# Kernel optimization log

Measured on AMD Instinct MI355X. Metric: run time of the kernel, lower is better.

Reference implementation:

```python
import jax, jax.numpy as jnp
import numpy as np

# Constants from the source's eval path
BBOX_STDS = (0.1, 0.1, 0.2, 0.2)   # cfg.TRAIN.BBOX_NORMALIZE_STDS (MEANS are zeros)
PRE_NMS = 300                       # cfg.TEST.RPN_POST_NMS_TOP_N
POST_K = 100                        # cfg.PERSON_NMS (fixed output size; zero-padded)
NMS_THRESH = 0.3
SCORE_THRESH = 0.05


def setup_inputs() -> dict:
    key = jax.random.key(0)
    k1, k2, k3, k4 = jax.random.split(key, 4)
    B, N = 64, 32768
    H = W = 1024.0
    # plausible RPN proposal boxes inside the image
    xy = jax.random.uniform(k1, (B, N, 2)) * (W - 160.0)
    wh = jax.random.uniform(k2, (B, N, 2)) * 120.0 + 8.0
    boxes = jnp.concatenate([xy, xy + wh], axis=-1)          # [B,N,4] x1y1x2y2
    cls_prob = jax.random.uniform(k3, (B, N, 2))              # softmax probs [bg, person]
    box_deltas = jax.random.normal(k4, (B, N, 4)) * 0.5
    im_info = jnp.tile(jnp.array([H, W, 1.0], jnp.float32), (B, 1))
    return {"cls_prob": cls_prob, "boxes": boxes, "box_deltas": box_deltas, "im_info": im_info}


def _decode_and_clip(boxes, deltas, im_info):
    # bbox_transform_inv with de-normalized deltas, then clip_boxes
    stds = jnp.array(BBOX_STDS, boxes.dtype)
    d = deltas * stds                                         # MEANS are zero
    w = boxes[..., 2] - boxes[..., 0] + 1.0
    h = boxes[..., 3] - boxes[..., 1] + 1.0
    cx = boxes[..., 0] + 0.5 * w
    cy = boxes[..., 1] + 0.5 * h
    pcx = d[..., 0] * w + cx
    pcy = d[..., 1] * h + cy
    pw = jnp.exp(d[..., 2]) * w
    ph = jnp.exp(d[..., 3]) * h
    x1 = pcx - 0.5 * pw
    y1 = pcy - 0.5 * ph
    x2 = pcx + 0.5 * pw
    y2 = pcy + 0.5 * ph
    hmax = im_info[:, 0][:, None] - 1.0   # [B,1]
    wmax = im_info[:, 1][:, None] - 1.0
    x1 = jnp.clip(x1, 0.0, wmax)
    y1 = jnp.clip(y1, 0.0, hmax)
    x2 = jnp.clip(x2, 0.0, wmax)
    y2 = jnp.clip(y2, 0.0, hmax)
    return jnp.stack([x1, y1, x2, y2], axis=-1)               # [B,N,4]


def _nms_single(boxes_i, scores_i):
    # threshold -> sort (top-k) -> greedy NMS -> fixed-size padded output
    valid = scores_i >= SCORE_THRESH
    s = jnp.where(valid, scores_i, -jnp.inf)
    topv, topi = jax.lax.top_k(s, PRE_NMS)                    # descending sort + pre_nms_topN
    b = boxes_i[topi]                                          # [M,4]
    x1, y1, x2, y2 = b[:, 0], b[:, 1], b[:, 2], b[:, 3]
    areas = (x2 - x1 + 1.0) * (y2 - y1 + 1.0)
    xx1 = jnp.maximum(x1[:, None], x1[None, :])
    yy1 = jnp.maximum(y1[:, None], y1[None, :])
    xx2 = jnp.minimum(x2[:, None], x2[None, :])
    yy2 = jnp.minimum(y2[:, None], y2[None, :])
    inter = jnp.maximum(xx2 - xx1 + 1.0, 0.0) * jnp.maximum(yy2 - yy1 + 1.0, 0.0)
    iou = inter / (areas[:, None] + areas[None, :] - inter)    # [M,M]
    iou = jax.lax.stop_gradient(iou)                           # only drives the boolean keep mask
    idx = jnp.arange(PRE_NMS)
    keep0 = jnp.isfinite(topv)                                 # drop below-threshold padding

    def body(i, keep):
        sup = (iou[i] > NMS_THRESH) & (idx > i) & keep[i]
        return keep & ~sup

    keep = jax.lax.fori_loop(0, PRE_NMS, body, keep0)
    # compact kept boxes (in score order) into a fixed [POST_K,4] buffer, zero-padded
    rank = jnp.cumsum(keep) - 1
    dst = jnp.where(keep & (rank < POST_K), rank, POST_K)      # overflow row POST_K is discarded
    out = jnp.zeros((POST_K + 1, 4), b.dtype).at[dst].set(b)
    return out[:POST_K]


def reference(cls_prob, boxes, box_deltas, im_info):
    pred = _decode_and_clip(boxes, box_deltas, im_info)        # [B,N,4]
    scores_person = cls_prob[:, :, 1]                          # person column
    kept = jax.vmap(_nms_single)(pred, scores_person)          # [B,POST_K,4]
    B = pred.shape[0]
    bidx = jnp.broadcast_to(jnp.arange(B, dtype=pred.dtype)[:, None, None], (B, POST_K, 1))
    return jnp.concatenate([bidx, kept], axis=-1)              # [B,POST_K,5] rois
```

## Files before the change

kernel.cpp:

```cpp
#include <hip/hip_runtime.h>
#include <cstdint>
#include <cstddef>

#define PRE_NMS  300
#define POST_K   100
#define NBUCKET  4096
#define CAND_MAX 2048
#define NCHUNK   16
#define SUB      128
#define NWORDS   5
#define SUP_STRIDE 6
#define NMS_T    0.3f
#define SCORE_T  0.05f
#define FAST_T   0.9875f

typedef unsigned long long u64;

__global__ __launch_bounds__(256) void scan_kernel(
    const float* __restrict__ cls_prob,
    u64* __restrict__ candG,
    int* __restrict__ cntG,
    int N)
{
    const int b     = blockIdx.x >> 4;
    const int chunk = blockIdx.x & (NCHUNK - 1);
    const int nq    = N / 2;
    const int per   = (nq + NCHUNK - 1) / NCHUNK;
    const int base  = chunk * per;
    const int end   = min(base + per, nq);

    __shared__ int lcnt;
    __shared__ u64 lbuf[SUB];
    if (threadIdx.x == 0) lcnt = 0;
    __syncthreads();

    const float4* cp = (const float4*)(cls_prob + (size_t)b * N * 2);
    for (int q = base + threadIdx.x; q < end; q += 256) {
        float4 v = cp[q];
        #pragma unroll
        for (int h = 0; h < 2; ++h) {
            float s = h ? v.w : v.y;
            if (s >= FAST_T) {
                int pos = atomicAdd(&lcnt, 1);
                if (pos < SUB) {
                    unsigned int m = __float_as_uint(s) ^ 0xFFFFFFFFu;
                    lbuf[pos] = ((u64)m << 32) | (unsigned int)(2 * q + h);
                }
            }
        }
    }
    __syncthreads();

    const int cnt = lcnt;
    u64* cb = candG + ((size_t)b * NCHUNK + chunk) * SUB;
    for (int i = threadIdx.x; i < min(cnt, SUB); i += 256) cb[i] = lbuf[i];
    if (threadIdx.x == 0) cntG[b * NCHUNK + chunk] = cnt;
}

__device__ __forceinline__ u64 keep_init_word(int Kv, int w) {
    int rem = Kv - 64 * w;
    if (rem >= 64) return ~0ull;
    if (rem <= 0)  return 0ull;
    return (1ull << rem) - 1ull;
}

__global__ __launch_bounds__(512) void proposal_kernel(
    const float* __restrict__ cls_prob,
    const float* __restrict__ boxes,
    const float* __restrict__ deltas,
    const float* __restrict__ im_info,
    float* __restrict__ out,
    const u64* __restrict__ candG,
    const int* __restrict__ cntG,
    int useWS, int N)
{
    const int b   = blockIdx.x;
    const int tid = threadIdx.x;
    const int NT  = 512;

    __shared__ u64 cand[CAND_MAX];
    int* hist = (int*)cand;
    __shared__ u64 skey[PRE_NMS];
    __shared__ float bx1[PRE_NMS], by1[PRE_NMS], bx2[PRE_NMS], by2[PRE_NMS], barea[PRE_NMS];
    __shared__ u64 supRow[PRE_NMS * SUP_STRIDE];
    __shared__ u64 keepw[NWORDS];
    __shared__ int sel[POST_K];
    __shared__ int n_out;
    __shared__ int sh_cc;
    __shared__ int sh_ok;
    __shared__ int cand_count;
    __shared__ int cutoff;
    __shared__ int ccnt[NCHUNK], coff[NCHUNK + 1];

    if (tid == 0) cand_count = 0;
    __syncthreads();

    const float4* cp = (const float4*)(cls_prob + (size_t)b * N * 2);
    const int nq = N / 2;

    if (useWS && tid < NCHUNK) ccnt[tid] = cntG[b * NCHUNK + tid];
    __syncthreads();
    if (tid == 0) {
        int ok = useWS;
        int tot = 0;
        if (useWS) {
            for (int c = 0; c < NCHUNK; ++c) {
                if (ccnt[c] > SUB) ok = 0;
                coff[c] = tot;
                tot += ccnt[c];
            }
            coff[NCHUNK] = tot;
            if (tot < PRE_NMS || tot > CAND_MAX) ok = 0;
        }
        sh_ok = ok;
        sh_cc = tot;
    }
    __syncthreads();
    const bool fast = (sh_ok != 0);
    int cc;

    if (fast) {
        cc = sh_cc;
        const int c = tid >> 5;
        const u64* cb = candG + ((size_t)b * NCHUNK + c) * SUB;
        const int n = ccnt[c], o = coff[c];
        for (int i = tid & 31; i < n; i += 32) cand[o + i] = cb[i];
    } else {
        for (int q = tid; q < nq; q += NT) {
            float4 v = cp[q];
            #pragma unroll
            for (int h = 0; h < 2; ++h) {
                float s = h ? v.w : v.y;
                if (s >= FAST_T) {
                    int pos = atomicAdd(&cand_count, 1);
                    if (pos < CAND_MAX) {
                        unsigned int m = __float_as_uint(s) ^ 0xFFFFFFFFu;
                        cand[pos] = ((u64)m << 32) | (unsigned int)(2 * q + h);
                    }
                }
            }
        }
        __syncthreads();
        if (cand_count < PRE_NMS) {
            for (int i = tid; i < NBUCKET; i += NT) hist[i] = 0;
            __syncthreads();
            for (int q = tid; q < nq; q += NT) {
                float4 v = cp[q];
                if (v.y >= SCORE_T) atomicAdd(&hist[min((int)(v.y * (float)NBUCKET), NBUCKET - 1)], 1);
                if (v.w >= SCORE_T) atomicAdd(&hist[min((int)(v.w * (float)NBUCKET), NBUCKET - 1)], 1);
            }
            __syncthreads();
            if (tid == 0) {
                int acc = 0, c = 0;
                for (int i = NBUCKET - 1; i >= 0; --i) {
                    acc += hist[i];
                    if (acc >= PRE_NMS) { c = i; break; }
                }
                cutoff = c;
                cand_count = 0;
            }
            __syncthreads();
            const int c = cutoff;
            for (int q = tid; q < nq; q += NT) {
                float4 v = cp[q];
                #pragma unroll
                for (int h = 0; h < 2; ++h) {
                    float s = h ? v.w : v.y;
                    if (s >= SCORE_T) {
                        int bu = min((int)(s * (float)NBUCKET), NBUCKET - 1);
                        if (bu >= c) {
                            int pos = atomicAdd(&cand_count, 1);
                            if (pos < CAND_MAX) {
                                unsigned int m = __float_as_uint(s) ^ 0xFFFFFFFFu;
                                cand[pos] = ((u64)m << 32) | (unsigned int)(2 * q + h);
                            }
                        }
                    }
                }
            }
            __syncthreads();
        }
        cc = min(cand_count, CAND_MAX);
        if (tid == 0) sh_cc = cc;
        __syncthreads();
        cc = sh_cc;
    }

    for (int k = tid; k < PRE_NMS; k += NT) skey[k] = ~0ull;
    __syncthreads();
    for (int c = tid; c < cc; c += NT) {
        u64 my = cand[c];
        int rank = 0;
        for (int k = 0; k < cc; ++k) rank += (cand[k] < my) ? 1 : 0;
        if (rank < PRE_NMS) skey[rank] = my;
    }
    __syncthreads();

    const int Kv = min(cc, PRE_NMS);

    const float hmax = im_info[b * 3 + 0] - 1.0f;
    const float wmax = im_info[b * 3 + 1] - 1.0f;
    if (tid < PRE_NMS) {
        int k = tid;
        int idx = (k < Kv) ? (int)(skey[k] & 0xFFFFFFFFull) : 0;
        float4 bo = *(const float4*)(boxes  + ((size_t)b * N + idx) * 4);
        float4 de = *(const float4*)(deltas + ((size_t)b * N + idx) * 4);
        float w  = bo.z - bo.x + 1.0f;
        float hh = bo.w - bo.y + 1.0f;
        float cx = bo.x + 0.5f * w;
        float cy = bo.y + 0.5f * hh;
        float dx = de.x * 0.1f, dy = de.y * 0.1f;
        float dw = de.z * 0.2f, dh = de.w * 0.2f;
        float pcx = dx * w + cx;
        float pcy = dy * hh + cy;
        float pw  = expf(dw) * w;
        float ph  = expf(dh) * hh;
        float x1 = pcx - 0.5f * pw, y1 = pcy - 0.5f * ph;
        float x2 = pcx + 0.5f * pw, y2 = pcy + 0.5f * ph;
        x1 = fminf(fmaxf(x1, 0.0f), wmax);
        y1 = fminf(fmaxf(y1, 0.0f), hmax);
        x2 = fminf(fmaxf(x2, 0.0f), wmax);
        y2 = fminf(fmaxf(y2, 0.0f), hmax);
        bx1[k] = x1; by1[k] = y1; bx2[k] = x2; by2[k] = y2;
        barea[k] = (x2 - x1 + 1.0f) * (y2 - y1 + 1.0f);
    }
    __syncthreads();

    for (int t = tid; t < PRE_NMS * NWORDS; t += NT) {
        int w = t / PRE_NMS;
        int i = t - w * PRE_NMS;
        int jbase = w * 64;
        int jend  = min(jbase + 64, PRE_NMS);
        u64 bits = 0;
        int jstart = max(jbase, i + 1);
        if (jstart < jend) {
            float xi1 = bx1[i], yi1 = by1[i], xi2 = bx2[i], yi2 = by2[i], ai = barea[i];
            for (int j = jstart; j < jend; ++j) {
                float xx1 = fmaxf(xi1, bx1[j]);
                float yy1 = fmaxf(yi1, by1[j]);
                float xx2 = fminf(xi2, bx2[j]);
                float yy2 = fminf(yi2, by2[j]);
                float iw = fmaxf(xx2 - xx1 + 1.0f, 0.0f);
                float ih = fmaxf(yy2 - yy1 + 1.0f, 0.0f);
                float inter = iw * ih;
                float iou = inter / (ai + barea[j] - inter);
                if (iou > NMS_T) bits |= (1ull << (j - jbase));
            }
        }
        supRow[i * SUP_STRIDE + w] = bits;
    }
    __syncthreads();

    if (tid < 64) {
        u64 kw0 = keep_init_word(Kv, 0);
        u64 kw1 = keep_init_word(Kv, 1);
        u64 kw2 = keep_init_word(Kv, 2);
        u64 kw3 = keep_init_word(Kv, 3);
        u64 kw4 = keep_init_word(Kv, 4);

        int nk = 0;
        #pragma unroll
        for (int wi = 0; wi < NWORDS; ++wi) {
            if (nk >= POST_K) break;
            u64 w = (wi == 0) ? kw0 : (wi == 1) ? kw1 : (wi == 2) ? kw2 : (wi == 3) ? kw3 : kw4;
            while (w != 0ull && nk < POST_K) {
                int bit = __ffsll(w) - 1;
                int i = wi * 64 + bit;
                const u64* r = supRow + i * SUP_STRIDE;
                u64 r0 = r[0], r1 = r[1], r2 = r[2], r3 = r[3], r4 = r[4];
                kw0 &= ~r0; kw1 &= ~r1; kw2 &= ~r2; kw3 &= ~r3; kw4 &= ~r4;
                ++nk;
                u64 self = (wi == 0) ? kw0 : (wi == 1) ? kw1 : (wi == 2) ? kw2 : (wi == 3) ? kw3 : kw4;
                u64 below = (bit == 63) ? ~0ull : ((1ull << (bit + 1)) - 1ull);
                w = self & ~below;
            }
        }
        if (tid == 0) {
            keepw[0] = kw0; keepw[1] = kw1; keepw[2] = kw2; keepw[3] = kw3; keepw[4] = kw4;
            n_out = nk;
        }
    }
    __syncthreads();

    if (tid < PRE_NMS) {
        int wi = tid >> 6, bi = tid & 63;
        u64 w = keepw[wi];
        int prefix = 0;
        #pragma unroll
        for (int ww = 0; ww < NWORDS; ++ww)
            if (ww < wi) prefix += __popcll(keepw[ww]);
        prefix += __popcll(w & ((1ull << bi) - 1ull));
        if (((w >> bi) & 1ull) && prefix < POST_K) sel[prefix] = tid;
    }
    __syncthreads();

    if (tid < POST_K) {
        float* op = out + ((size_t)b * POST_K + tid) * 5;
        op[0] = (float)b;
        if (tid < n_out) {
            int k = sel[tid];
            op[1] = bx1[k]; op[2] = by1[k]; op[3] = bx2[k]; op[4] = by2[k];
        } else {
            op[1] = 0.0f; op[2] = 0.0f; op[3] = 0.0f; op[4] = 0.0f;
        }
    }
}

extern "C" void kernel_launch(void* const* d_in, const int* in_sizes, int n_in,
                              void* d_out, int out_size, void* d_ws, size_t ws_size,
                              hipStream_t stream) {
    const float* cls_prob = (const float*)d_in[0];
    const float* boxes    = (const float*)d_in[1];
    const float* deltas   = (const float*)d_in[2];
    const float* im_info  = (const float*)d_in[3];
    float* out = (float*)d_out;

    const int B = in_sizes[3] / 3;
    const int N = in_sizes[0] / (B * 2);

    int* cntG   = (int*)d_ws;
    u64* candG  = (u64*)((char*)d_ws + 16384);
    size_t need = 16384 + (size_t)B * NCHUNK * SUB * sizeof(u64);
    int useWS   = (ws_size >= need && B * NCHUNK * (int)sizeof(int) <= 16384) ? 1 : 0;

    if (useWS) {
        scan_kernel<<<B * NCHUNK, 256, 0, stream>>>(cls_prob, candG, cntG, N);
    }
    proposal_kernel<<<B, 512, 0, stream>>>(cls_prob, boxes, deltas, im_info, out,
                                           candG, cntG, useWS, N);
}
```

Measured before the change: 142.4 us.

## Fuse rank sort with box decode and pack boxes as float4 in shared memory

Each candidate thread now issues its global box and delta loads before computing its rank, then decodes and writes the clipped box straight to its ranked slot. This removes the skey staging array, a barrier, and a separate dependent gather phase, and overlaps the load latency with the rank loop. Boxes are stored as one float4 array, with areas recomputed on the fly instead of kept in a separate array, and the suppression row stride is padded to 8. The cost is that every candidate, not just the top PRE_NMS, loads its box data, and the IoU inner loop does extra area arithmetic.

```diff
diff --git a/kernel.cpp b/kernel.cpp
--- a/kernel.cpp
+++ b/kernel.cpp
@@ -9,7 +9,7 @@
 #define NCHUNK   16
 #define SUB      128
 #define NWORDS   5
-#define SUP_STRIDE 6
+#define SUP_STRIDE 8
 #define NMS_T    0.3f
 #define SCORE_T  0.05f
 #define FAST_T   0.9875f
@@ -80,8 +80,7 @@
 
     __shared__ u64 cand[CAND_MAX];
     int* hist = (int*)cand;
-    __shared__ u64 skey[PRE_NMS];
-    __shared__ float bx1[PRE_NMS], by1[PRE_NMS], bx2[PRE_NMS], by2[PRE_NMS], barea[PRE_NMS];
+    __shared__ float4 bb[PRE_NMS];
     __shared__ u64 supRow[PRE_NMS * SUP_STRIDE];
     __shared__ u64 keepw[NWORDS];
     __shared__ int sel[POST_K];
@@ -186,43 +185,35 @@
         cc = sh_cc;
     }
 
-    for (int k = tid; k < PRE_NMS; k += NT) skey[k] = ~0ull;
-    __syncthreads();
+    for (int k = tid; k < PRE_NMS; k += NT) bb[k] = make_float4(0.f, 0.f, 0.f, 0.f);
+    __syncthreads();
+
+    const int Kv = min(cc, PRE_NMS);
+
+    const float hmax = im_info[b * 3 + 0] - 1.0f;
+    const float wmax = im_info[b * 3 + 1] - 1.0f;
     for (int c = tid; c < cc; c += NT) {
         u64 my = cand[c];
+        int idx = (int)(my & 0xFFFFFFFFull);
+        float4 bo = *(const float4*)(boxes  + ((size_t)b * N + idx) * 4);
+        float4 de = *(const float4*)(deltas + ((size_t)b * N + idx) * 4);
         int rank = 0;
         for (int k = 0; k < cc; ++k) rank += (cand[k] < my) ? 1 : 0;
-        if (rank < PRE_NMS) skey[rank] = my;
-    }
-    __syncthreads();
-
-    const int Kv = min(cc, PRE_NMS);
-
-    const float hmax = im_info[b * 3 + 0] - 1.0f;
-    const float wmax = im_info[b * 3 + 1] - 1.0f;
-    if (tid < PRE_NMS) {
-        int k = tid;
-        int idx = (k < Kv) ? (int)(skey[k] & 0xFFFFFFFFull) : 0;
-        float4 bo = *(const float4*)(boxes  + ((size_t)b * N + idx) * 4);
-        float4 de = *(const float4*)(deltas + ((size_t)b * N + idx) * 4);
-        float w  = bo.z - bo.x + 1.0f;
-        float hh = bo.w - bo.y + 1.0f;
-        float cx = bo.x + 0.5f * w;
-        float cy = bo.y + 0.5f * hh;
-        float dx = de.x * 0.1f, dy = de.y * 0.1f;
-        float dw = de.z * 0.2f, dh = de.w * 0.2f;
-        float pcx = dx * w + cx;
-        float pcy = dy * hh + cy;
-        float pw  = expf(dw) * w;
-        float ph  = expf(dh) * hh;
-        float x1 = pcx - 0.5f * pw, y1 = pcy - 0.5f * ph;
-        float x2 = pcx + 0.5f * pw, y2 = pcy + 0.5f * ph;
-        x1 = fminf(fmaxf(x1, 0.0f), wmax);
-        y1 = fminf(fmaxf(y1, 0.0f), hmax);
-        x2 = fminf(fmaxf(x2, 0.0f), wmax);
-        y2 = fminf(fmaxf(y2, 0.0f), hmax);
-        bx1[k] = x1; by1[k] = y1; bx2[k] = x2; by2[k] = y2;
-        barea[k] = (x2 - x1 + 1.0f) * (y2 - y1 + 1.0f);
+        if (rank < PRE_NMS) {
+            float w  = bo.z - bo.x + 1.0f;
+            float hh = bo.w - bo.y + 1.0f;
+            float cx = bo.x + 0.5f * w;
+            float cy = bo.y + 0.5f * hh;
+            float pcx = de.x * 0.1f * w + cx;
+            float pcy = de.y * 0.1f * hh + cy;
+            float pw  = expf(de.z * 0.2f) * w;
+            float ph  = expf(de.w * 0.2f) * hh;
+            float x1 = fminf(fmaxf(pcx - 0.5f * pw, 0.0f), wmax);
+            float y1 = fminf(fmaxf(pcy - 0.5f * ph, 0.0f), hmax);
+            float x2 = fminf(fmaxf(pcx + 0.5f * pw, 0.0f), wmax);
+            float y2 = fminf(fmaxf(pcy + 0.5f * ph, 0.0f), hmax);
+            bb[rank] = make_float4(x1, y1, x2, y2);
+        }
     }
     __syncthreads();
 
@@ -234,16 +225,19 @@
         u64 bits = 0;
         int jstart = max(jbase, i + 1);
         if (jstart < jend) {
-            float xi1 = bx1[i], yi1 = by1[i], xi2 = bx2[i], yi2 = by2[i], ai = barea[i];
+            float4 bi = bb[i];
+            float ai = (bi.z - bi.x + 1.0f) * (bi.w - bi.y + 1.0f);
             for (int j = jstart; j < jend; ++j) {
-                float xx1 = fmaxf(xi1, bx1[j]);
-                float yy1 = fmaxf(yi1, by1[j]);
-                float xx2 = fminf(xi2, bx2[j]);
-                float yy2 = fminf(yi2, by2[j]);
+                float4 bj = bb[j];
+                float aj = (bj.z - bj.x + 1.0f) * (bj.w - bj.y + 1.0f);
+                float xx1 = fmaxf(bi.x, bj.x);
+                float yy1 = fmaxf(bi.y, bj.y);
+                float xx2 = fminf(bi.z, bj.z);
+                float yy2 = fminf(bi.w, bj.w);
                 float iw = fmaxf(xx2 - xx1 + 1.0f, 0.0f);
                 float ih = fmaxf(yy2 - yy1 + 1.0f, 0.0f);
                 float inter = iw * ih;
-                float iou = inter / (ai + barea[j] - inter);
+                float iou = inter / (ai + aj - inter);
                 if (iou > NMS_T) bits |= (1ull << (j - jbase));
             }
         }
@@ -298,8 +292,8 @@
         float* op = out + ((size_t)b * POST_K + tid) * 5;
         op[0] = (float)b;
         if (tid < n_out) {
-            int k = sel[tid];
-            op[1] = bx1[k]; op[2] = by1[k]; op[3] = bx2[k]; op[4] = by2[k];
+            float4 v = bb[sel[tid]];
+            op[1] = v.x; op[2] = v.y; op[3] = v.z; op[4] = v.w;
         } else {
             op[1] = 0.0f; op[2] = 0.0f; op[3] = 0.0f; op[4] = 0.0f;
         }
```

New measurement: 140.9 us. No clear change (-1.1%).
